# Kernel tuning notes

Hardware: AMD Instinct MI355X
Metric: run time of the kernel (lower is better)

## Reference

```python
import jax, jax.numpy as jnp
import numpy as np

B, F, E = 4096, 39, 16
FIELD_DIMS = [1000] * F
OFFSETS = jnp.asarray(np.concatenate([[0], np.cumsum(FIELD_DIMS)[:-1]]).astype(np.int64))
I_IDX, J_IDX = np.triu_indices(F, 1)  # 741 pairs (i<j)
I_IDX = jnp.asarray(I_IDX); J_IDX = jnp.asarray(J_IDX)
MLP_DIMS = [2 * 741 * E, 400, 400, 400]
EPS = 1e-5


def setup_inputs() -> dict:
    key = jax.random.key(0)
    ks = jax.random.split(key, 20)
    s = 0.02
    inp = {
        'x': jax.random.randint(ks[0], (B, F), 0, 1000, dtype=jnp.int64),
        'emb': jax.random.normal(ks[1], (sum(FIELD_DIMS), E), jnp.float32) * s,
        'sen_w1': jax.random.normal(ks[2], (F, F), jnp.float32) * s,
        'sen_b1': jnp.zeros((F,), jnp.float32),
        'sen_w2': jax.random.normal(ks[3], (F, F), jnp.float32) * s,
        'sen_b2': jnp.zeros((F,), jnp.float32),
        'Wb1': jax.random.normal(ks[4], (E, E), jnp.float32) * s,
        'Wb2': jax.random.normal(ks[5], (E, E), jnp.float32) * s,
    }
    for li in range(3):
        din, dout = MLP_DIMS[li], MLP_DIMS[li + 1]
        inp[f'mw{li}'] = jax.random.normal(ks[6 + li], (dout, din), jnp.float32) * s
        inp[f'mb{li}'] = jnp.zeros((dout,), jnp.float32)
        inp[f'g{li}'] = jnp.ones((dout,), jnp.float32)
        inp[f'be{li}'] = jnp.zeros((dout,), jnp.float32)
    inp['mw3'] = jax.random.normal(ks[9], (1, MLP_DIMS[-1]), jnp.float32) * s
    inp['mb3'] = jnp.zeros((1,), jnp.float32)
    return inp


def _bilinear_all(v, W):
    # v: [B,F,E]; p_ij = (v_i W^T) * v_j for all i<j -> [B, P*E]
    proj = jnp.einsum('bfe,de->bfd', v, W)
    p = proj[:, I_IDX] * v[:, J_IDX]  # [B, 741, E]
    return p.reshape(v.shape[0], -1)


def _bn(h, g, be):
    mu = h.mean(axis=0)
    var = h.var(axis=0)
    return g * (h - mu) * jax.lax.rsqrt(var + EPS) + be


def _forward(x, emb, sen_w1, sen_b1, sen_w2, sen_b2, Wb1, Wb2,
             mw0, mb0, g0, be0, mw1, mb1, g1, be1, mw2, mb2, g2, be2, mw3, mb3):
    xe = emb[x + OFFSETS[None, :]]  # [B,F,E]
    # SENet: max over embed dim, two-layer excitation with ReLU
    z = jnp.max(xe, axis=2)  # [B,F]
    a = jax.nn.relu(jax.nn.relu(z @ sen_w1.T + sen_b1) @ sen_w2.T + sen_b2)  # [B,F]
    x_sen = a[:, :, None] * xe
    x_con = jnp.concatenate([_bilinear_all(xe, Wb1), _bilinear_all(x_sen, Wb2)], axis=1)
    h = x_con
    for w, b, g, be in ((mw0, mb0, g0, be0), (mw1, mb1, g1, be1), (mw2, mb2, g2, be2)):
        h = jax.nn.relu(_bn(h @ w.T + b, g, be))  # dropout = identity (eval)
    return h @ mw3.T + mb3  # [B,1]


def reference(x, emb, sen_w1, sen_b1, sen_w2, sen_b2, Wb1, Wb2,
              mw0, mb0, g0, be0, mw1, mb1, g1, be1, mw2, mb2, g2, be2, mw3, mb3):
    return _forward(x, emb, sen_w1, sen_b1, sen_w2, sen_b2, Wb1, Wb2,
                    mw0, mb0, g0, be0, mw1, mb1, g1, be1, mw2, mb2, g2, be2, mw3, mb3)
```

## Files before the change

kernel.cpp:

```cpp
#include <hip/hip_runtime.h>
#include <stdint.h>

#define B_ROWS  4096
#define F_FIELDS 39
#define NPAIR   741
#define XCON_K  23712
#define KP      23744
#define NP      512
#define HID     400
#define SPLITK0 8
#define KITERS0 (KP/64)

#define OFF_XCON 0ull
#define SZ_XCON  ((size_t)B_ROWS * KP * 2)
#define OFF_W0B  (OFF_XCON + SZ_XCON)
#define SZ_W0B   ((size_t)NP * KP * 2)
#define OFF_W1B  (OFF_W0B + SZ_W0B)
#define SZ_WSM   ((size_t)NP * NP * 2)
#define OFF_W2B  (OFF_W1B + SZ_WSM)
#define OFF_HPRE (OFF_W2B + SZ_WSM)
#define SZ_HPRE  ((size_t)B_ROWS * NP * 4)
#define OFF_HN   (OFF_HPRE + SZ_HPRE)
#define SZ_HN    ((size_t)B_ROWS * NP * 2)
#define OFF_STATS (OFF_HN + SZ_HN)
#define SZ_STATS  (6 * 512 * 4)
#define WS_NEEDED (OFF_STATS + SZ_STATS + 4096)

__device__ __forceinline__ unsigned short f2bf(float f) {
    union { float f; unsigned u; } v; v.f = f;
    unsigned r = (v.u + 0x7FFFu + ((v.u >> 16) & 1u)) >> 16;
    return (unsigned short)r;
}
__device__ __forceinline__ void gl_lds16(const void* g, void* l) {
    __builtin_amdgcn_global_load_lds(
        (const __attribute__((address_space(1))) void*)g,
        (__attribute__((address_space(3))) void*)l, 16, 0, 0);
}

typedef __bf16 bf16x8 __attribute__((ext_vector_type(8)));
typedef float  floatx4 __attribute__((ext_vector_type(4)));

__global__ __launch_bounds__(256) void build_all(
    const int* __restrict__ x, const float* __restrict__ emb,
    const float* __restrict__ w1, const float* __restrict__ b1,
    const float* __restrict__ w2, const float* __restrict__ b2,
    const float* __restrict__ Wb1, const float* __restrict__ Wb2,
    unsigned short* __restrict__ xcon,
    const float* __restrict__ mw0, unsigned short* __restrict__ w0b,
    const float* __restrict__ mw1, const float* __restrict__ mw2,
    unsigned short* __restrict__ w1b, unsigned short* __restrict__ w2b)
{
    __shared__ float xe[624], pp[2][624];
    __shared__ float zz[40], tt[40], aa[40];
    __shared__ short itab[NPAIR], jtab[NPAIR];
    const int bb = blockIdx.x, tid = threadIdx.x;

    if (bb >= B_ROWS) {
        if (bb < B_ROWS + NP) {
            const int o = bb - B_ROWS;
            for (int k4 = tid; k4 < KP / 4; k4 += 256) {
                const int k = k4 * 4;
                unsigned short u[4] = {0, 0, 0, 0};
                if (o < HID && k < XCON_K) {
                    float4 v = *(const float4*)&mw0[(size_t)o * XCON_K + k];
                    u[0] = f2bf(v.x); u[1] = f2bf(v.y); u[2] = f2bf(v.z); u[3] = f2bf(v.w);
                }
                uint2 pk; pk.x = u[0] | ((unsigned)u[1] << 16); pk.y = u[2] | ((unsigned)u[3] << 16);
                *(uint2*)&w0b[(size_t)o * KP + k] = pk;
            }
        } else {
            const int idx = bb - B_ROWS - NP;
            const int which = idx >> 9;
            const int o = idx & 511;
            const float* w = which ? mw2 : mw1;
            unsigned short* o_ = which ? w2b : w1b;
            for (int k = tid; k < NP; k += 256) {
                float v = (o < HID && k < HID) ? w[o * HID + k] : 0.f;
                o_[o * NP + k] = f2bf(v);
            }
        }
        return;
    }

    const int b = bb;
    for (int p = tid; p < NPAIR; p += 256) {
        float fp = (float)p;
        int i = (int)(38.5f - sqrtf(38.5f * 38.5f - 2.f * fp));
        while (i > 0 && p < (i * (77 - i)) / 2) --i;
        while (p >= ((i + 1) * (76 - i)) / 2) ++i;
        itab[p] = (short)i;
        jtab[p] = (short)(i + 1 + (p - (i * (77 - i)) / 2));
    }
    if (tid < 156) {
        int f = tid >> 2, e4 = (tid & 3) * 4;
        int row = x[b * F_FIELDS + f] + 1000 * f;
        *(float4*)&xe[f * 16 + e4] = *(const float4*)&emb[row * 16 + e4];
    }
    __syncthreads();
    if (tid < F_FIELDS) {
        float m = xe[tid * 16];
        for (int e = 1; e < 16; ++e) m = fmaxf(m, xe[tid * 16 + e]);
        zz[tid] = m;
    }
    __syncthreads();
    if (tid < F_FIELDS) {
        float s = b1[tid];
        for (int g = 0; g < F_FIELDS; ++g) s += zz[g] * w1[tid * F_FIELDS + g];
        tt[tid] = fmaxf(s, 0.f);
    }
    __syncthreads();
    if (tid < F_FIELDS) {
        float s = b2[tid];
        for (int g = 0; g < F_FIELDS; ++g) s += tt[g] * w2[tid * F_FIELDS + g];
        aa[tid] = fmaxf(s, 0.f);
    }
    __syncthreads();
    for (int idx = tid; idx < 624; idx += 256) {
        int f = idx >> 4, d = idx & 15;
        float s1 = 0.f, s2 = 0.f;
        for (int e = 0; e < 16; ++e) {
            float v = xe[f * 16 + e];
            s1 += v * Wb1[d * 16 + e];
            s2 += v * Wb2[d * 16 + e];
        }
        pp[0][idx] = s1; pp[1][idx] = s2;
    }
    __syncthreads();
    unsigned short* out = xcon + (size_t)b * KP;
    for (int c = tid; c < 1484; c += 256) {
        if (c < 2 * NPAIR) {
            const int half = (c >= NPAIR);
            const int p = c - NPAIR * half;
            const int i = itab[p], j = jtab[p];
            const float f = half ? aa[i] * aa[j] : 1.f;
            const float* pr = &pp[half][i * 16];
            const float* xr = &xe[j * 16];
            unsigned short u[16];
#pragma unroll
            for (int e = 0; e < 16; ++e) u[e] = f2bf(f * pr[e] * xr[e]);
            uint4 v0, v1;
            v0.x = u[0] | ((unsigned)u[1] << 16);  v0.y = u[2] | ((unsigned)u[3] << 16);
            v0.z = u[4] | ((unsigned)u[5] << 16);  v0.w = u[6] | ((unsigned)u[7] << 16);
            v1.x = u[8] | ((unsigned)u[9] << 16);  v1.y = u[10] | ((unsigned)u[11] << 16);
            v1.z = u[12] | ((unsigned)u[13] << 16); v1.w = u[14] | ((unsigned)u[15] << 16);
            uint4* dst = (uint4*)(out + (half ? 11856 : 0) + p * 16);
            dst[0] = v0; dst[1] = v1;
        } else {
            uint4 z; z.x = z.y = z.z = z.w = 0u;
            ((uint4*)(out + XCON_K))[c - 2 * NPAIR] = z;
        }
    }
}

__global__ __launch_bounds__(256, 2) void gemm0(
    const unsigned short* __restrict__ A, const unsigned short* __restrict__ Bm,
    float* __restrict__ C, int kcnt)
{
    __shared__ __align__(16) unsigned short As[128 * 64];
    __shared__ __align__(16) unsigned short Bs[256 * 64];
    const int tid = threadIdx.x;
    const int m0 = blockIdx.y * 128, n0 = blockIdx.x * 256;
    int kb = blockIdx.z * kcnt;
    int ke = kb + kcnt; if (ke > KITERS0) ke = KITERS0;

    const int swz = (((tid & 7) ^ ((tid >> 3) & 7)) * 8);
    const unsigned short* Ag = A + (size_t)(m0 + (tid >> 3)) * KP + swz;
    const unsigned short* Bg = Bm + (size_t)(n0 + (tid >> 3)) * KP + swz;
    unsigned short* Asl = As + tid * 8;
    unsigned short* Bsl = Bs + tid * 8;

    const int wv = tid >> 6, ln = tid & 63;
    const int wm = (wv >> 1) * 64, wn = (wv & 1) * 128;
    const int l15 = ln & 15, lq = ln >> 4;
    const int xorm = l15 & 7;

    floatx4 acc[4][8];
#pragma unroll
    for (int mi = 0; mi < 4; ++mi)
#pragma unroll
        for (int ni = 0; ni < 8; ++ni)
            acc[mi][ni] = (floatx4){0.f, 0.f, 0.f, 0.f};

    for (int kt = kb; kt < ke; ++kt) {
        const size_t ko = (size_t)kt * 64;
#pragma unroll
        for (int i = 0; i < 4; ++i)
            gl_lds16(Ag + (size_t)(i * 32) * KP + ko, Asl + i * 2048);
#pragma unroll
        for (int i = 0; i < 8; ++i)
            gl_lds16(Bg + (size_t)(i * 32) * KP + ko, Bsl + i * 2048);
        __syncthreads();
#pragma unroll
        for (int kk = 0; kk < 64; kk += 32) {
            bf16x8 af[4], bfr[8];
#pragma unroll
            for (int t = 0; t < 4; ++t)
                af[t] = *(const bf16x8*)(As + (wm + t * 16 + l15) * 64
                                            + ((((kk >> 3) + lq) ^ xorm) * 8));
#pragma unroll
            for (int t = 0; t < 8; ++t)
                bfr[t] = *(const bf16x8*)(Bs + (wn + t * 16 + l15) * 64
                                             + ((((kk >> 3) + lq) ^ xorm) * 8));
#pragma unroll
            for (int mi = 0; mi < 4; ++mi)
#pragma unroll
                for (int ni = 0; ni < 8; ++ni)
                    acc[mi][ni] = __builtin_amdgcn_mfma_f32_16x16x32_bf16(
                        af[mi], bfr[ni], acc[mi][ni], 0, 0, 0);
        }
        __syncthreads();
    }
#pragma unroll
    for (int mi = 0; mi < 4; ++mi)
#pragma unroll
        for (int ni = 0; ni < 8; ++ni) {
            const int col = n0 + wn + ni * 16 + l15;
            const int row0 = m0 + wm + mi * 16 + lq * 4;
#pragma unroll
            for (int r = 0; r < 4; ++r)
                atomicAdd(&C[(size_t)(row0 + r) * NP + col], acc[mi][ni][r]);
        }
}

__global__ __launch_bounds__(256) void gemm_small(
    const unsigned short* __restrict__ A, const unsigned short* __restrict__ Bm,
    float* __restrict__ C, float* __restrict__ cs, float* __restrict__ csq)
{
    __shared__ __align__(16) unsigned short As[64 * 64];
    __shared__ __align__(16) unsigned short Bs[64 * 64];
    const int tid = threadIdx.x;
    const int m0 = blockIdx.y * 64, n0 = blockIdx.x * 64;

    const int swz = (((tid & 7) ^ ((tid >> 3) & 7)) * 8);
    const unsigned short* Ag = A + (size_t)(m0 + (tid >> 3)) * NP + swz;
    const unsigned short* Bg = Bm + (size_t)(n0 + (tid >> 3)) * NP + swz;
    unsigned short* Asl = As + tid * 8;
    unsigned short* Bsl = Bs + tid * 8;

    const int wv = tid >> 6, ln = tid & 63;
    const int wm = (wv >> 1) * 32, wn = (wv & 1) * 32;
    const int l15 = ln & 15, lq = ln >> 4;
    const int xorm = l15 & 7;

    floatx4 acc[2][2];
#pragma unroll
    for (int mi = 0; mi < 2; ++mi)
#pragma unroll
        for (int ni = 0; ni < 2; ++ni)
            acc[mi][ni] = (floatx4){0.f, 0.f, 0.f, 0.f};

    for (int kt = 0; kt < NP / 64; ++kt) {
        const size_t ko = (size_t)kt * 64;
#pragma unroll
        for (int i = 0; i < 2; ++i) {
            gl_lds16(Ag + (size_t)(i * 32) * NP + ko, Asl + i * 2048);
            gl_lds16(Bg + (size_t)(i * 32) * NP + ko, Bsl + i * 2048);
        }
        __syncthreads();
#pragma unroll
        for (int kk = 0; kk < 64; kk += 32) {
            bf16x8 af[2], bfr[2];
#pragma unroll
            for (int t = 0; t < 2; ++t) {
                af[t]  = *(const bf16x8*)(As + (wm + t * 16 + l15) * 64
                                             + ((((kk >> 3) + lq) ^ xorm) * 8));
                bfr[t] = *(const bf16x8*)(Bs + (wn + t * 16 + l15) * 64
                                             + ((((kk >> 3) + lq) ^ xorm) * 8));
            }
#pragma unroll
            for (int mi = 0; mi < 2; ++mi)
#pragma unroll
                for (int ni = 0; ni < 2; ++ni)
                    acc[mi][ni] = __builtin_amdgcn_mfma_f32_16x16x32_bf16(
                        af[mi], bfr[ni], acc[mi][ni], 0, 0, 0);
        }
        __syncthreads();
    }
#pragma unroll
    for (int mi = 0; mi < 2; ++mi)
#pragma unroll
        for (int ni = 0; ni < 2; ++ni) {
            const int col = n0 + wn + ni * 16 + l15;
            const int row0 = m0 + wm + mi * 16 + lq * 4;
#pragma unroll
            for (int r = 0; r < 4; ++r)
                C[(size_t)(row0 + r) * NP + col] = acc[mi][ni][r];
        }
#pragma unroll
    for (int ni = 0; ni < 2; ++ni) {
        float s = 0.f, q = 0.f;
#pragma unroll
        for (int mi = 0; mi < 2; ++mi)
#pragma unroll
            for (int r = 0; r < 4; ++r) { float v = acc[mi][ni][r]; s += v; q += v * v; }
        s += __shfl_down(s, 32); q += __shfl_down(q, 32);
        s += __shfl_down(s, 16); q += __shfl_down(q, 16);
        if (lq == 0) {
            const int col = n0 + wn + ni * 16 + l15;
            atomicAdd(&cs[col], s);
            atomicAdd(&csq[col], q);
        }
    }
}

__global__ __launch_bounds__(256) void colstats(const float* __restrict__ H,
                                                float* __restrict__ cs, float* __restrict__ csq) {
    const int tid = threadIdx.x;
    const int c4 = (tid & 127) * 4;
    const int ro = tid >> 7;
    const int r0 = blockIdx.x * 32;
    float s0 = 0, s1 = 0, s2 = 0, s3 = 0, q0 = 0, q1 = 0, q2 = 0, q3 = 0;
#pragma unroll
    for (int i = 0; i < 16; ++i) {
        float4 v = *(const float4*)&H[(size_t)(r0 + ro + 2 * i) * NP + c4];
        s0 += v.x; q0 += v.x * v.x;  s1 += v.y; q1 += v.y * v.y;
        s2 += v.z; q2 += v.z * v.z;  s3 += v.w; q3 += v.w * v.w;
    }
    atomicAdd(&cs[c4], s0); atomicAdd(&cs[c4 + 1], s1);
    atomicAdd(&cs[c4 + 2], s2); atomicAdd(&cs[c4 + 3], s3);
    atomicAdd(&csq[c4], q0); atomicAdd(&csq[c4 + 1], q1);
    atomicAdd(&csq[c4 + 2], q2); atomicAdd(&csq[c4 + 3], q3);
}

__global__ __launch_bounds__(256) void bnrelu(const float* __restrict__ H,
                       const float* __restrict__ cs, const float* __restrict__ csq,
                       const float* __restrict__ g, const float* __restrict__ be,
                       unsigned short* __restrict__ O) {
    __shared__ float sc[NP], sh[NP];
    for (int c = threadIdx.x; c < NP; c += 256) {
        float mean = cs[c] * (1.f / 4096.f);
        float var  = csq[c] * (1.f / 4096.f) - mean * mean;
        float s = (c < HID ? g[c] : 0.f) * rsqrtf(var + 1e-5f);
        sc[c] = s;
        sh[c] = (c < HID ? be[c] : 0.f) - mean * s;
    }
    __syncthreads();
    const size_t n4 = (size_t)B_ROWS * NP / 4;
    const size_t stride = (size_t)gridDim.x * 256;
    for (size_t i = (size_t)blockIdx.x * 256 + threadIdx.x; i < n4; i += stride) {
        const int c = (int)(i & 127) * 4;
        float4 v = ((const float4*)H)[i];
        unsigned short u0 = f2bf(fmaxf(v.x * sc[c]     + sh[c],     0.f));
        unsigned short u1 = f2bf(fmaxf(v.y * sc[c + 1] + sh[c + 1], 0.f));
        unsigned short u2 = f2bf(fmaxf(v.z * sc[c + 2] + sh[c + 2], 0.f));
        unsigned short u3 = f2bf(fmaxf(v.w * sc[c + 3] + sh[c + 3], 0.f));
        uint2 pk; pk.x = u0 | ((unsigned)u1 << 16); pk.y = u2 | ((unsigned)u3 << 16);
        *(uint2*)&O[i * 4] = pk;
    }
}

__global__ __launch_bounds__(256) void bnrelu_dot(const float* __restrict__ H,
                       const float* __restrict__ cs, const float* __restrict__ csq,
                       const float* __restrict__ g, const float* __restrict__ be,
                       const float* __restrict__ w3, const float* __restrict__ b3,
                       float* __restrict__ out) {
    __shared__ float sc[NP], sh[NP], ww[NP];
    for (int c = threadIdx.x; c < NP; c += 256) {
        float mean = cs[c] * (1.f / 4096.f);
        float var  = csq[c] * (1.f / 4096.f) - mean * mean;
        float s = (c < HID ? g[c] : 0.f) * rsqrtf(var + 1e-5f);
        sc[c] = s;
        sh[c] = (c < HID ? be[c] : 0.f) - mean * s;
        ww[c] = (c < HID ? w3[c] : 0.f);
    }
    __syncthreads();
    const int wv = threadIdx.x >> 6, ln = threadIdx.x & 63;
    const int row = blockIdx.x * 4 + wv;
    const float4* hp = (const float4*)(H + (size_t)row * NP);
    float s = 0.f;
#pragma unroll
    for (int it = 0; it < 2; ++it) {
        const int c4 = it * 64 + ln;
        const int c = c4 * 4;
        float4 v = hp[c4];
        s += fmaxf(v.x * sc[c]     + sh[c],     0.f) * ww[c]
           + fmaxf(v.y * sc[c + 1] + sh[c + 1], 0.f) * ww[c + 1]
           + fmaxf(v.z * sc[c + 2] + sh[c + 2], 0.f) * ww[c + 2]
           + fmaxf(v.w * sc[c + 3] + sh[c + 3], 0.f) * ww[c + 3];
    }
#pragma unroll
    for (int o = 32; o; o >>= 1) s += __shfl_down(s, o);
    if (ln == 0) out[row] = s + b3[0];
}

extern "C" void kernel_launch(void* const* d_in, const int* in_sizes, int n_in,
                              void* d_out, int out_size, void* d_ws, size_t ws_size,
                              hipStream_t stream)
{
    const int*   x    = (const int*)d_in[0];
    const float* emb  = (const float*)d_in[1];
    const float* sw1  = (const float*)d_in[2];
    const float* sb1  = (const float*)d_in[3];
    const float* sw2  = (const float*)d_in[4];
    const float* sb2  = (const float*)d_in[5];
    const float* Wb1  = (const float*)d_in[6];
    const float* Wb2  = (const float*)d_in[7];
    const float* mw0  = (const float*)d_in[8];
    const float* g0   = (const float*)d_in[10];
    const float* be0  = (const float*)d_in[11];
    const float* mw1  = (const float*)d_in[12];
    const float* g1   = (const float*)d_in[14];
    const float* be1  = (const float*)d_in[15];
    const float* mw2  = (const float*)d_in[16];
    const float* g2   = (const float*)d_in[18];
    const float* be2  = (const float*)d_in[19];
    const float* mw3  = (const float*)d_in[20];
    const float* mb3  = (const float*)d_in[21];
    (void)in_sizes; (void)n_in; (void)out_size;
    if (ws_size < WS_NEEDED) return;

    char* ws = (char*)d_ws;
    unsigned short* xcon = (unsigned short*)(ws + OFF_XCON);
    unsigned short* w0b  = (unsigned short*)(ws + OFF_W0B);
    unsigned short* w1b  = (unsigned short*)(ws + OFF_W1B);
    unsigned short* w2b  = (unsigned short*)(ws + OFF_W2B);
    float* hpre = (float*)(ws + OFF_HPRE);
    unsigned short* hn = (unsigned short*)(ws + OFF_HN);
    float* stats = (float*)(ws + OFF_STATS);
    float* cs0 = stats,        *csq0 = stats + 512;
    float* cs1 = stats + 1024, *csq1 = stats + 1536;
    float* cs2 = stats + 2048, *csq2 = stats + 2560;

    build_all<<<B_ROWS + NP + 2 * NP, 256, 0, stream>>>(
        x, emb, sw1, sb1, sw2, sb2, Wb1, Wb2, xcon, mw0, w0b, mw1, mw2, w1b, w2b);

    hipMemsetAsync(hpre, 0, SZ_HPRE, stream);
    hipMemsetAsync(stats, 0, SZ_STATS, stream);

    gemm0<<<dim3(NP / 256, B_ROWS / 128, SPLITK0), 256, 0, stream>>>(
        xcon, w0b, hpre, (KITERS0 + SPLITK0 - 1) / SPLITK0);
    colstats<<<128, 256, 0, stream>>>(hpre, cs0, csq0);
    bnrelu<<<512, 256, 0, stream>>>(hpre, cs0, csq0, g0, be0, hn);

    gemm_small<<<dim3(NP / 64, B_ROWS / 64), 256, 0, stream>>>(hn, w1b, hpre, cs1, csq1);
    bnrelu<<<512, 256, 0, stream>>>(hpre, cs1, csq1, g1, be1, hn);

    gemm_small<<<dim3(NP / 64, B_ROWS / 64), 256, 0, stream>>>(hn, w2b, hpre, cs2, csq2);
    bnrelu_dot<<<B_ROWS / 4, 256, 0, stream>>>(hpre, cs2, csq2, g2, be2, mw3, mb3, (float*)d_out);
}
```

Baseline: 377.8 us.

## Fuse BN+ReLU into small GEMM prologue and raise split-K for first GEMM

Removes the standalone bnrelu kernels by applying batch-norm scale/shift and ReLU while loading the A tile in the small GEMMs, so the normalized activations are never written out and read back. The middle layer's pre-activation is stored as bf16, which halves that intermediate's traffic but rounds the values before normalization. Split-K for the large first GEMM goes from 8 to 12 and its occupancy hint from 2 to 3 blocks per CU, giving more parallelism at the cost of more atomic adds. The A tile now goes through registers instead of direct global-to-LDS loads, which may lengthen the small GEMMs' load phase.

```diff
diff --git a/kernel.cpp b/kernel.cpp
--- a/kernel.cpp
+++ b/kernel.cpp
@@ -8,7 +8,7 @@
 #define KP      23744
 #define NP      512
 #define HID     400
-#define SPLITK0 8
+#define SPLITK0 12
 #define KITERS0 (KP/64)
 
 #define OFF_XCON 0ull
@@ -30,6 +30,10 @@
     union { float f; unsigned u; } v; v.f = f;
     unsigned r = (v.u + 0x7FFFu + ((v.u >> 16) & 1u)) >> 16;
     return (unsigned short)r;
+}
+__device__ __forceinline__ float bf2f(unsigned short h) {
+    union { unsigned u; float f; } v; v.u = ((unsigned)h) << 16;
+    return v.f;
 }
 __device__ __forceinline__ void gl_lds16(const void* g, void* l) {
     __builtin_amdgcn_global_load_lds(
@@ -152,7 +156,7 @@
     }
 }
 
-__global__ __launch_bounds__(256, 2) void gemm0(
+__global__ __launch_bounds__(256, 3) void gemm0(
     const unsigned short* __restrict__ A, const unsigned short* __restrict__ Bm,
     float* __restrict__ C, int kcnt)
 {
@@ -222,19 +226,30 @@
         }
 }
 
-__global__ __launch_bounds__(256) void gemm_small(
-    const unsigned short* __restrict__ A, const unsigned short* __restrict__ Bm,
-    float* __restrict__ C, float* __restrict__ cs, float* __restrict__ csq)
+template<int MODE>
+__global__ __launch_bounds__(256) void gemm_bn(
+    const void* __restrict__ Ain, const unsigned short* __restrict__ Bm,
+    const float* __restrict__ cs, const float* __restrict__ csq,
+    const float* __restrict__ g, const float* __restrict__ be,
+    void* __restrict__ Cout, float* __restrict__ csO, float* __restrict__ csqO)
 {
     __shared__ __align__(16) unsigned short As[64 * 64];
     __shared__ __align__(16) unsigned short Bs[64 * 64];
+    __shared__ float sc[NP], sh[NP];
     const int tid = threadIdx.x;
     const int m0 = blockIdx.y * 64, n0 = blockIdx.x * 64;
 
-    const int swz = (((tid & 7) ^ ((tid >> 3) & 7)) * 8);
-    const unsigned short* Ag = A + (size_t)(m0 + (tid >> 3)) * NP + swz;
-    const unsigned short* Bg = Bm + (size_t)(n0 + (tid >> 3)) * NP + swz;
-    unsigned short* Asl = As + tid * 8;
+    for (int c = tid; c < NP; c += 256) {
+        float mean = cs[c] * (1.f / 4096.f);
+        float var  = csq[c] * (1.f / 4096.f) - mean * mean;
+        float s = (c < HID ? g[c] : 0.f) * rsqrtf(var + 1e-5f);
+        sc[c] = s;
+        sh[c] = (c < HID ? be[c] : 0.f) - mean * s;
+    }
+
+    const int r = tid >> 3, c8 = tid & 7;
+    const int gsw = c8 ^ (r & 7);
+    const unsigned short* Bg = Bm + (size_t)(n0 + r) * NP + gsw * 8;
     unsigned short* Bsl = Bs + tid * 8;
 
     const int wv = tid >> 6, ln = tid & 63;
@@ -249,13 +264,49 @@
         for (int ni = 0; ni < 2; ++ni)
             acc[mi][ni] = (floatx4){0.f, 0.f, 0.f, 0.f};
 
+    __syncthreads();
+
     for (int kt = 0; kt < NP / 64; ++kt) {
-        const size_t ko = (size_t)kt * 64;
+        const int ko = kt * 64;
+        const int kc = ko + gsw * 8;
 #pragma unroll
         for (int i = 0; i < 2; ++i) {
-            gl_lds16(Ag + (size_t)(i * 32) * NP + ko, Asl + i * 2048);
+            const int row = m0 + r + i * 32;
+            unsigned short u[8];
+            if (MODE == 0) {
+                const float* ap = (const float*)Ain + (size_t)row * NP + kc;
+                float4 v0 = *(const float4*)ap;
+                float4 v1 = *(const float4*)(ap + 4);
+                u[0] = f2bf(fmaxf(v0.x * sc[kc]     + sh[kc],     0.f));
+                u[1] = f2bf(fmaxf(v0.y * sc[kc + 1] + sh[kc + 1], 0.f));
+                u[2] = f2bf(fmaxf(v0.z * sc[kc + 2] + sh[kc + 2], 0.f));
+                u[3] = f2bf(fmaxf(v0.w * sc[kc + 3] + sh[kc + 3], 0.f));
+                u[4] = f2bf(fmaxf(v1.x * sc[kc + 4] + sh[kc + 4], 0.f));
+                u[5] = f2bf(fmaxf(v1.y * sc[kc + 5] + sh[kc + 5], 0.f));
+                u[6] = f2bf(fmaxf(v1.z * sc[kc + 6] + sh[kc + 6], 0.f));
+                u[7] = f2bf(fmaxf(v1.w * sc[kc + 7] + sh[kc + 7], 0.f));
+            } else {
+                const unsigned short* ap = (const unsigned short*)Ain + (size_t)row * NP + kc;
+                uint4 pk = *(const uint4*)ap;
+                unsigned short raw[8] = {
+                    (unsigned short)(pk.x & 0xFFFF), (unsigned short)(pk.x >> 16),
+                    (unsigned short)(pk.y & 0xFFFF), (unsigned short)(pk.y >> 16),
+                    (unsigned short)(pk.z & 0xFFFF), (unsigned short)(pk.z >> 16),
+                    (unsigned short)(pk.w & 0xFFFF), (unsigned short)(pk.w >> 16)};
+#pragma unroll
+                for (int e = 0; e < 8; ++e)
+                    u[e] = f2bf(fmaxf(bf2f(raw[e]) * sc[kc + e] + sh[kc + e], 0.f));
+            }
+            uint4 w;
+            w.x = u[0] | ((unsigned)u[1] << 16);
+            w.y = u[2] | ((unsigned)u[3] << 16);
+            w.z = u[4] | ((unsigned)u[5] << 16);
+            w.w = u[6] | ((unsigned)u[7] << 16);
+            *(uint4*)(As + (r + i * 32) * 64 + c8 * 8) = w;
+        }
+#pragma unroll
+        for (int i = 0; i < 2; ++i)
             gl_lds16(Bg + (size_t)(i * 32) * NP + ko, Bsl + i * 2048);
-        }
         __syncthreads();
 #pragma unroll
         for (int kk = 0; kk < 64; kk += 32) {
@@ -283,8 +334,12 @@
             const int col = n0 + wn + ni * 16 + l15;
             const int row0 = m0 + wm + mi * 16 + lq * 4;
 #pragma unroll
-            for (int r = 0; r < 4; ++r)
-                C[(size_t)(row0 + r) * NP + col] = acc[mi][ni][r];
+            for (int rr = 0; rr < 4; ++rr) {
+                if (MODE == 0)
+                    ((unsigned short*)Cout)[(size_t)(row0 + rr) * NP + col] = f2bf(acc[mi][ni][rr]);
+                else
+                    ((float*)Cout)[(size_t)(row0 + rr) * NP + col] = acc[mi][ni][rr];
+            }
         }
 #pragma unroll
     for (int ni = 0; ni < 2; ++ni) {
@@ -292,13 +347,13 @@
 #pragma unroll
         for (int mi = 0; mi < 2; ++mi)
 #pragma unroll
-            for (int r = 0; r < 4; ++r) { float v = acc[mi][ni][r]; s += v; q += v * v; }
+            for (int rr = 0; rr < 4; ++rr) { float v = acc[mi][ni][rr]; s += v; q += v * v; }
         s += __shfl_down(s, 32); q += __shfl_down(q, 32);
         s += __shfl_down(s, 16); q += __shfl_down(q, 16);
         if (lq == 0) {
             const int col = n0 + wn + ni * 16 + l15;
-            atomicAdd(&cs[col], s);
-            atomicAdd(&csq[col], q);
+            atomicAdd(&csO[col], s);
+            atomicAdd(&csqO[col], q);
         }
     }
 }
@@ -320,33 +375,6 @@
     atomicAdd(&cs[c4 + 2], s2); atomicAdd(&cs[c4 + 3], s3);
     atomicAdd(&csq[c4], q0); atomicAdd(&csq[c4 + 1], q1);
     atomicAdd(&csq[c4 + 2], q2); atomicAdd(&csq[c4 + 3], q3);
-}
-
-__global__ __launch_bounds__(256) void bnrelu(const float* __restrict__ H,
-                       const float* __restrict__ cs, const float* __restrict__ csq,
-                       const float* __restrict__ g, const float* __restrict__ be,
-                       unsigned short* __restrict__ O) {
-    __shared__ float sc[NP], sh[NP];
-    for (int c = threadIdx.x; c < NP; c += 256) {
-        float mean = cs[c] * (1.f / 4096.f);
-        float var  = csq[c] * (1.f / 4096.f) - mean * mean;
-        float s = (c < HID ? g[c] : 0.f) * rsqrtf(var + 1e-5f);
-        sc[c] = s;
-        sh[c] = (c < HID ? be[c] : 0.f) - mean * s;
-    }
-    __syncthreads();
-    const size_t n4 = (size_t)B_ROWS * NP / 4;
-    const size_t stride = (size_t)gridDim.x * 256;
-    for (size_t i = (size_t)blockIdx.x * 256 + threadIdx.x; i < n4; i += stride) {
-        const int c = (int)(i & 127) * 4;
-        float4 v = ((const float4*)H)[i];
-        unsigned short u0 = f2bf(fmaxf(v.x * sc[c]     + sh[c],     0.f));
-        unsigned short u1 = f2bf(fmaxf(v.y * sc[c + 1] + sh[c + 1], 0.f));
-        unsigned short u2 = f2bf(fmaxf(v.z * sc[c + 2] + sh[c + 2], 0.f));
-        unsigned short u3 = f2bf(fmaxf(v.w * sc[c + 3] + sh[c + 3], 0.f));
-        uint2 pk; pk.x = u0 | ((unsigned)u1 << 16); pk.y = u2 | ((unsigned)u3 << 16);
-        *(uint2*)&O[i * 4] = pk;
-    }
 }
 
 __global__ __launch_bounds__(256) void bnrelu_dot(const float* __restrict__ H,
@@ -430,11 +458,12 @@
     gemm0<<<dim3(NP / 256, B_ROWS / 128, SPLITK0), 256, 0, stream>>>(
         xcon, w0b, hpre, (KITERS0 + SPLITK0 - 1) / SPLITK0);
     colstats<<<128, 256, 0, stream>>>(hpre, cs0, csq0);
-    bnrelu<<<512, 256, 0, stream>>>(hpre, cs0, csq0, g0, be0, hn);
-
-    gemm_small<<<dim3(NP / 64, B_ROWS / 64), 256, 0, stream>>>(hn, w1b, hpre, cs1, csq1);
-    bnrelu<<<512, 256, 0, stream>>>(hpre, cs1, csq1, g1, be1, hn);
-
-    gemm_small<<<dim3(NP / 64, B_ROWS / 64), 256, 0, stream>>>(hn, w2b, hpre, cs2, csq2);
+
+    gemm_bn<0><<<dim3(NP / 64, B_ROWS / 64), 256, 0, stream>>>(
+        hpre, w1b, cs0, csq0, g0, be0, hn, cs1, csq1);
+
+    gemm_bn<1><<<dim3(NP / 64, B_ROWS / 64), 256, 0, stream>>>(
+        hn, w2b, cs1, csq1, g1, be1, hpre, cs2, csq2);
+
     bnrelu_dot<<<B_ROWS / 4, 256, 0, stream>>>(hpre, cs2, csq2, g2, be2, mw3, mb3, (float*)d_out);
 }
```

New measurement: 489.9 us. 1.3x slower.
